# Performance work log

Measured on AMD Instinct MI355X. Metric: run time of the kernel, lower is better.

The kernel has to match this reference:

```python
import jax, jax.numpy as jnp
import numpy as np

D = 4096
N_HEAD = 32
KV_HEAD = 8
GS = D * KV_HEAD // N_HEAD  # 1024, kv projection width
B, S = 1, 2048


def setup_inputs() -> dict:
    key = jax.random.key(0)
    ks = jax.random.split(key, 10)
    sc = 0.02
    return {
        "x": jax.random.normal(ks[0], (B, S, D), dtype=jnp.float32),
        "y": jax.random.normal(ks[1], (B, S, D), dtype=jnp.float32),
        "Wq": jax.random.normal(ks[2], (D, D), dtype=jnp.float32) * sc,
        "bq": jax.random.normal(ks[3], (D,), dtype=jnp.float32) * sc,
        "Wk": jax.random.normal(ks[4], (D, GS), dtype=jnp.float32) * sc,
        "bk": jax.random.normal(ks[5], (GS,), dtype=jnp.float32) * sc,
        "Wv": jax.random.normal(ks[6], (D, GS), dtype=jnp.float32) * sc,
        "bv": jax.random.normal(ks[7], (GS,), dtype=jnp.float32) * sc,
        "Wo": jax.random.normal(ks[8], (D, D), dtype=jnp.float32) * sc,
        "bo": jax.random.normal(ks[9], (D,), dtype=jnp.float32) * sc,
        "n_head": N_HEAD,
        "kv_head": KV_HEAD,
    }


def reference(x, y, Wq, bq, Wk, bk, Wv, bv, Wo, bo, n_head, kv_head):
    b, s, d = x.shape
    hd = d // n_head              # per-head dim
    gvs = hd // 2                 # complex pairs per head (group_vector_size)
    q = (x @ Wq + bq).reshape(b, s, n_head, hd)
    k = (y @ Wk + bk).reshape(b, s, kv_head, hd)
    v = (y @ Wv + bv).reshape(b, s, kv_head, hd)

    # RoPE: phi = 1/5000**(i/gvs); angle[p, i] = phi[i] * p  (matrix.T in torch)
    phi = 1.0 / (5000.0 ** (jnp.arange(gvs, dtype=jnp.float32) / gvs))
    ang = jnp.arange(s, dtype=jnp.float32)[:, None] * phi[None, :]  # [S, gvs]
    cos = jnp.cos(ang)[None, :, None, :]  # [1,S,1,gvs]
    sin = jnp.sin(ang)[None, :, None, :]

    def rope(t):
        # interleaved pairs (t[...,2i], t[...,2i+1]) form complex numbers
        tr, ti = t[..., 0::2], t[..., 1::2]
        ro = tr * cos - ti * sin
        io = tr * sin + ti * cos
        return jnp.stack([ro, io], axis=-1).reshape(t.shape)

    q = rope(q)
    k = rope(k)

    # GQA: head h uses kv head h // (n_head // kv_head) -> repeat kv heads
    module = n_head // kv_head
    k = jnp.repeat(k, module, axis=2)  # [B,S,H,hd]
    v = jnp.repeat(v, module, axis=2)

    scores = jnp.einsum("bqhd,bkhd->bhqk", q, k) / jnp.sqrt(jnp.float32(hd))
    causal = jnp.tril(jnp.ones((s, s), dtype=bool))
    scores = jnp.where(causal[None, None], scores, -jnp.inf)
    attn = jax.nn.softmax(scores, axis=-1)
    out = jnp.einsum("bhqk,bkhd->bqhd", attn, v).reshape(b, s, d)
    return out @ Wo + bo
```

## Files before the change

### kernel.cpp

```cpp
#include <hip/hip_runtime.h>
#include <hip/hip_bf16.h>

typedef unsigned int uint32;
typedef unsigned short ushort16;
typedef __attribute__((ext_vector_type(8))) __bf16 bf16x8;
typedef __attribute__((ext_vector_type(4))) float f32x4;

__device__ __forceinline__ ushort16 f2bf(float f) {
    uint32 u = __float_as_uint(f);
    u += 0x7fff + ((u >> 16) & 1);
    return (ushort16)(u >> 16);
}
__device__ __forceinline__ uint32 pack2rn(float a, float b) {
    uint32 ua = __float_as_uint(a) + 0x8000u;
    uint32 ub = __float_as_uint(b) + 0x8000u;
    return __builtin_amdgcn_perm(ub, ua, 0x07060302);
}
__device__ __forceinline__ float blo(uint32 u) { return __uint_as_float(u << 16); }
__device__ __forceinline__ float bhi(uint32 u) { return __uint_as_float(u & 0xffff0000u); }

__device__ __forceinline__ void storeC(float v, float* p) { *p = v; }
__device__ __forceinline__ void storeC(float v, ushort16* p) { *p = f2bf(v); }

__device__ __forceinline__ void gload_lds16(const void* g, void* l) {
    __builtin_amdgcn_global_load_lds(
        (const __attribute__((address_space(1))) unsigned int*)g,
        (__attribute__((address_space(3))) unsigned int*)l, 16, 0, 0);
}

__global__ __launch_bounds__(256) void conv_bf16(
    const float* __restrict__ X, ushort16* __restrict__ Xb, int n8)
{
    int idx = blockIdx.x * blockDim.x + threadIdx.x;
    if (idx >= n8) return;
    float4 a = ((const float4*)X)[2 * idx];
    float4 b = ((const float4*)X)[2 * idx + 1];
    uint4 u;
    u.x = pack2rn(a.x, a.y); u.y = pack2rn(a.z, a.w);
    u.z = pack2rn(b.x, b.y); u.w = pack2rn(b.z, b.w);
    ((uint4*)Xb)[idx] = u;
}

__global__ __launch_bounds__(256) void transpose_w_bf16(
    const float* __restrict__ W, ushort16* __restrict__ Wt, int N)
{
    __shared__ float tile[64][65];
    const int k0 = blockIdx.x * 64, n0 = blockIdx.y * 64;
#pragma unroll
    for (int it = 0; it < 16; ++it) {
        int idx = threadIdx.x + it * 256;
        int r = idx >> 6, c = idx & 63;
        tile[r][c] = W[(size_t)(k0 + r) * N + n0 + c];
    }
    __syncthreads();
#pragma unroll
    for (int it = 0; it < 8; ++it) {
        int idx = threadIdx.x + it * 256;
        int nr = idx >> 5, kp = idx & 31;
        uint32 u = pack2rn(tile[2 * kp][nr], tile[2 * kp + 1][nr]);
        *(uint32*)&Wt[(size_t)(n0 + nr) * 4096 + k0 + 2 * kp] = u;
    }
}

template <typename OutT>
__global__ __launch_bounds__(256) void gemm_mfma(
    const ushort16* __restrict__ A, const ushort16* __restrict__ B,
    const float* __restrict__ b1, const float* __restrict__ b2,
    OutT* __restrict__ C, int N, int K, int nsplit)
{
    __shared__ __align__(16) ushort16 As[128 * 64];
    __shared__ __align__(16) ushort16 Bs[128 * 64];

    const int tid  = threadIdx.x;
    const int lane = tid & 63, wave = tid >> 6;
    const int quad = lane >> 4, m16 = lane & 15;
    const int wm = (wave >> 1) * 64, wn = (wave & 1) * 64;
    const int gm0 = blockIdx.y * 128, gn0 = blockIdx.x * 128;

    f32x4 acc[4][4];
#pragma unroll
    for (int i = 0; i < 4; ++i)
#pragma unroll
        for (int j = 0; j < 4; ++j) acc[i][j] = (f32x4){0.f, 0.f, 0.f, 0.f};

    const int rl = lane >> 3, cl = lane & 7;
    const int clog = cl ^ (rl & 7);
    const ushort16* Ag = A + (size_t)(gm0 + wave * 32 + rl) * K + clog * 8;
    const ushort16* Bg = B + (size_t)(gn0 + wave * 32 + rl) * K + clog * 8;
    char* AsW = (char*)As + wave * 4096;
    char* BsW = (char*)Bs + wave * 4096;

    for (int k0 = 0; k0 < K; k0 += 64) {
        __syncthreads();
#pragma unroll
        for (int i = 0; i < 4; ++i) {
            gload_lds16(Ag + (size_t)(8 * i) * K, AsW + i * 1024);
            gload_lds16(Bg + (size_t)(8 * i) * K, BsW + i * 1024);
        }
        Ag += 64; Bg += 64;
        __syncthreads();

#pragma unroll
        for (int s = 0; s < 2; ++s) {
            bf16x8 aF[4], bF[4];
            const int cr = s * 4 + quad;
#pragma unroll
            for (int i = 0; i < 4; ++i) {
                int r = wm + i * 16 + m16;
                aF[i] = *(const bf16x8*)&As[r * 64 + ((cr ^ (r & 7)) * 8)];
                int n = wn + i * 16 + m16;
                bF[i] = *(const bf16x8*)&Bs[n * 64 + ((cr ^ (n & 7)) * 8)];
            }
            __builtin_amdgcn_s_setprio(1);
#pragma unroll
            for (int i = 0; i < 4; ++i)
#pragma unroll
                for (int j = 0; j < 4; ++j)
                    acc[i][j] = __builtin_amdgcn_mfma_f32_16x16x32_bf16(
                        aF[i], bF[j], acc[i][j], 0, 0, 0);
            __builtin_amdgcn_s_setprio(0);
        }
    }

#pragma unroll
    for (int j = 0; j < 4; ++j) {
        int col = gn0 + wn + j * 16 + m16;
        float bb = (col < nsplit) ? b1[col] : b2[col - nsplit];
#pragma unroll
        for (int i = 0; i < 4; ++i) {
            int row0 = gm0 + wm + i * 16 + quad * 4;
#pragma unroll
            for (int r = 0; r < 4; ++r)
                storeC(acc[i][j][r] + bb, C + (size_t)(row0 + r) * N + col);
        }
    }
}

__global__ void rope_q_kernel(const float* __restrict__ T,
                              ushort16* __restrict__ Qb, int S)
{
    int idx = blockIdx.x * blockDim.x + threadIdx.x;
    if (idx >= S * 32 * 64) return;
    int i   = idx & 63;
    int rem = idx >> 6;
    int s   = rem >> 5;
    float inv = powf(5000.0f, -(float)i / 64.0f);
    float ang = (float)s * inv;
    float cs = cosf(ang), sn = sinf(ang);
    const float sc = 0.08838834764831845f * 1.4426950408889634f;
    size_t base = (size_t)rem * 128 + 2 * i;
    float tr = T[base], ti = T[base + 1];
    *(uint32*)&Qb[base] = pack2rn((tr * cs - ti * sn) * sc,
                                  (tr * sn + ti * cs) * sc);
}

__global__ void rope_k_kernel(ushort16* __restrict__ KVb, int S)
{
    int idx = blockIdx.x * blockDim.x + threadIdx.x;
    if (idx >= S * 8 * 64) return;
    int i   = idx & 63;
    int rem = idx >> 6;
    int s   = rem >> 3, h = rem & 7;
    float inv = powf(5000.0f, -(float)i / 64.0f);
    float ang = (float)s * inv;
    float cs = cosf(ang), sn = sinf(ang);
    uint32* p = (uint32*)&KVb[(size_t)s * 2048 + h * 128 + 2 * i];
    uint32 u = *p;
    float tr = blo(u), ti = bhi(u);
    *p = pack2rn(tr * cs - ti * sn, tr * sn + ti * cs);
}

__global__ __launch_bounds__(256) void flash_attn_kernel(
    const ushort16* __restrict__ Qb, const ushort16* __restrict__ KVb,
    ushort16* __restrict__ O)
{
    __shared__ __align__(16) ushort16 Ks[64 * 128];
    __shared__ __align__(16) ushort16 Vt[128 * 64];
    __shared__ __align__(16) ushort16 Ps[64 * 64];

    const int tid  = threadIdx.x;
    const int lane = tid & 63, wave = tid >> 6;
    const int quad = lane >> 4, m16 = lane & 15;
    const int h = (int)blockIdx.y, kvh = h >> 2;

    const ushort16* Kbase = KVb + kvh * 128;
    const ushort16* Vbase = KVb + 1024 + kvh * 128;

    for (int pass = 0; pass < 2; ++pass) {
        const int qi = pass ? (int)blockIdx.x : 31 - (int)blockIdx.x;
        const int q0 = qi * 64;

        bf16x8 qa[4];
        {
            const ushort16* qp = Qb + (size_t)(q0 + wave * 16 + m16) * 4096
                               + h * 128 + quad * 8;
#pragma unroll
            for (int ks = 0; ks < 4; ++ks)
                qa[ks] = *(const bf16x8*)(qp + ks * 32);
        }

        f32x4 acc_o[8];
#pragma unroll
        for (int t = 0; t < 8; ++t) acc_o[t] = (f32x4){0.f, 0.f, 0.f, 0.f};
        float m_i[4], l_i[4];
#pragma unroll
        for (int r = 0; r < 4; ++r) { m_i[r] = -1e30f; l_i[r] = 0.f; }

        for (int k0 = 0; k0 <= q0; k0 += 64) {
            __syncthreads();

#pragma unroll
            for (int it = 0; it < 4; ++it) {
                int idx = tid + it * 256;
                int row = idx >> 4, c = idx & 15;
                *(uint4*)&Ks[row * 128 + ((c ^ (row & 7)) * 8)] =
                    *(const uint4*)(Kbase + (size_t)(k0 + row) * 2048 + c * 8);
            }
#pragma unroll
            for (int it = 0; it < 2; ++it) {
                int idx = tid + it * 256;
                int rp  = idx & 31;
                int dcb = (idx >> 5) * 8;
                const ushort16* p0 = Vbase + (size_t)(k0 + 2 * rp) * 2048 + dcb;
                uint4 a = *(const uint4*)p0;
                uint4 b = *(const uint4*)(p0 + 2048);
                uint32 aw[4] = {a.x, a.y, a.z, a.w}, bw[4] = {b.x, b.y, b.z, b.w};
                int cc = rp >> 2, cbase = 2 * (rp & 3);
#pragma unroll
                for (int t = 0; t < 4; ++t) {
                    int d0 = dcb + 2 * t, d1 = d0 + 1;
                    *(uint32*)&Vt[d0 * 64 + ((cc ^ (d0 & 7)) * 8) + cbase] =
                        __builtin_amdgcn_perm(bw[t], aw[t], 0x05040100);
                    *(uint32*)&Vt[d1 * 64 + ((cc ^ (d1 & 7)) * 8) + cbase] =
                        __builtin_amdgcn_perm(bw[t], aw[t], 0x07060302);
                }
            }
            __syncthreads();

            f32x4 sacc[4];
#pragma unroll
            for (int j = 0; j < 4; ++j) sacc[j] = (f32x4){0.f, 0.f, 0.f, 0.f};
            __builtin_amdgcn_s_setprio(1);
#pragma unroll
            for (int ks = 0; ks < 4; ++ks) {
#pragma unroll
                for (int j = 0; j < 4; ++j) {
                    int n = j * 16 + m16;
                    bf16x8 kb = *(const bf16x8*)&Ks[n * 128 + (((ks * 4 + quad) ^ (n & 7)) * 8)];
                    sacc[j] = __builtin_amdgcn_mfma_f32_16x16x32_bf16(qa[ks], kb, sacc[j], 0, 0, 0);
                }
            }
            __builtin_amdgcn_s_setprio(0);

            if (k0 == q0) {
                int qr = wave * 16 + quad * 4;
#pragma unroll
                for (int j = 0; j < 4; ++j) {
                    int kvl = j * 16 + m16;
#pragma unroll
                    for (int r = 0; r < 4; ++r)
                        if (kvl > qr + r) sacc[j][r] = -1e30f;
                }
            }

#pragma unroll
            for (int r = 0; r < 4; ++r) {
                float rm = fmaxf(fmaxf(sacc[0][r], sacc[1][r]), fmaxf(sacc[2][r], sacc[3][r]));
                rm = fmaxf(rm, __shfl_xor(rm, 1));
                rm = fmaxf(rm, __shfl_xor(rm, 2));
                rm = fmaxf(rm, __shfl_xor(rm, 4));
                rm = fmaxf(rm, __shfl_xor(rm, 8));
                float mnew = fmaxf(m_i[r], rm);
                float al = exp2f(m_i[r] - mnew);
                float rs = 0.f;
#pragma unroll
                for (int j = 0; j < 4; ++j) {
                    float pv = exp2f(sacc[j][r] - mnew);
                    sacc[j][r] = pv;
                    rs += pv;
                }
                rs += __shfl_xor(rs, 1);
                rs += __shfl_xor(rs, 2);
                rs += __shfl_xor(rs, 4);
                rs += __shfl_xor(rs, 8);
                l_i[r] = l_i[r] * al + rs;
                m_i[r] = mnew;
                int q = wave * 16 + quad * 4 + r;
#pragma unroll
                for (int j = 0; j < 4; ++j) {
                    int kv = j * 16 + m16;
                    Ps[q * 64 + (((kv >> 3) ^ (q & 7)) * 8) + (kv & 7)] = f2bf(sacc[j][r]);
                }
#pragma unroll
                for (int t = 0; t < 8; ++t) acc_o[t][r] *= al;
            }

            int qrow = wave * 16 + m16;
#pragma unroll
            for (int ks2 = 0; ks2 < 2; ++ks2) {
                bf16x8 pa = *(const bf16x8*)&Ps[qrow * 64 + (((ks2 * 4 + quad) ^ (qrow & 7)) * 8)];
                __builtin_amdgcn_s_setprio(1);
#pragma unroll
                for (int t = 0; t < 8; ++t) {
                    int d = t * 16 + m16;
                    bf16x8 vb = *(const bf16x8*)&Vt[d * 64 + (((ks2 * 4 + quad) ^ (d & 7)) * 8)];
                    acc_o[t] = __builtin_amdgcn_mfma_f32_16x16x32_bf16(pa, vb, acc_o[t], 0, 0, 0);
                }
                __builtin_amdgcn_s_setprio(0);
            }
        }

        ushort16* op = O + (size_t)(q0 + wave * 16 + quad * 4) * 4096 + h * 128 + m16;
#pragma unroll
        for (int r = 0; r < 4; ++r) {
            float inv = 1.0f / l_i[r];
#pragma unroll
            for (int t = 0; t < 8; ++t)
                op[(size_t)r * 4096 + t * 16] = f2bf(acc_o[t][r] * inv);
        }
    }
}

extern "C" void kernel_launch(void* const* d_in, const int* in_sizes, int n_in,
                              void* d_out, int out_size, void* d_ws, size_t ws_size,
                              hipStream_t stream)
{
    const float* x  = (const float*)d_in[0];
    const float* y  = (const float*)d_in[1];
    const float* Wq = (const float*)d_in[2];
    const float* bq = (const float*)d_in[3];
    const float* Wk = (const float*)d_in[4];
    const float* bk = (const float*)d_in[5];
    const float* Wv = (const float*)d_in[6];
    const float* bv = (const float*)d_in[7];
    const float* Wo = (const float*)d_in[8];
    const float* bo = (const float*)d_in[9];
    float* out = (float*)d_out;

    const int S = 2048, D = 4096;
    const size_t MB = 1024 * 1024;

    char* ws = (char*)d_ws;
    ushort16* xb   = (ushort16*)(ws);
    ushort16* yb   = (ushort16*)(ws + 16 * MB);
    ushort16* Wqt  = (ushort16*)(ws + 32 * MB);
    ushort16* Wkvt = (ushort16*)(ws + 64 * MB);
    ushort16* Wot  = (ushort16*)(ws + 80 * MB);
    ushort16* KVb  = (ushort16*)(ws + 112 * MB);
    ushort16* Qb   = xb;
    ushort16* Ao   = yb;
    float*    Q    = out;

    const int n8 = S * D / 8;
    conv_bf16<<<n8 / 256, 256, 0, stream>>>(x, xb, n8);
    conv_bf16<<<n8 / 256, 256, 0, stream>>>(y, yb, n8);
    transpose_w_bf16<<<dim3(64, 64), 256, 0, stream>>>(Wq, Wqt, D);
    transpose_w_bf16<<<dim3(64, 16), 256, 0, stream>>>(Wk, Wkvt, 1024);
    transpose_w_bf16<<<dim3(64, 16), 256, 0, stream>>>(Wv, Wkvt + (size_t)1024 * 4096, 1024);
    transpose_w_bf16<<<dim3(64, 64), 256, 0, stream>>>(Wo, Wot, D);

    gemm_mfma<float><<<dim3(32, 16), 256, 0, stream>>>(
        xb, Wqt, bq, bq, Q, D, D, D);
    gemm_mfma<ushort16><<<dim3(16, 16), 256, 0, stream>>>(
        yb, Wkvt, bk, bv, KVb, 2048, D, 1024);

    rope_q_kernel<<<(S * 32 * 64 + 255) / 256, 256, 0, stream>>>(Q, Qb, S);
    rope_k_kernel<<<(S * 8 * 64 + 255) / 256, 256, 0, stream>>>(KVb, S);

    flash_attn_kernel<<<dim3(16, 32), 256, 0, stream>>>(Qb, KVb, Ao);

    gemm_mfma<float><<<dim3(32, 16), 256, 0, stream>>>(
        Ao, Wot, bo, bo, out, D, D, D);
}
```

Baseline: 664.9 us.

## Merge prep, QKV GEMM and RoPE launches; one query tile per attention block

Merges the x/y bf16 conversion into one launch and the Wq/Wk/Wv transposes into one launch. Replaces the separate Q and KV projection GEMMs with a single gemm_qkv launch that picks its operands by block index, and fuses the Q and K RoPE kernels into one. This removes launch gaps and lets the smaller KV GEMM share a wave with the Q GEMM. Flash attention now does one query tile per block on a 32x32 grid instead of two paired tiles per block on 16x32. That doubles the block count but drops the paired load balancing, so causal work per block becomes uneven.

```diff
diff --git a/kernel.cpp b/kernel.cpp
--- a/kernel.cpp
+++ b/kernel.cpp
@@ -28,24 +28,35 @@
         (__attribute__((address_space(3))) unsigned int*)l, 16, 0, 0);
 }
 
-__global__ __launch_bounds__(256) void conv_bf16(
-    const float* __restrict__ X, ushort16* __restrict__ Xb, int n8)
+__global__ __launch_bounds__(256) void conv2_bf16(
+    const float* __restrict__ X, const float* __restrict__ Y,
+    ushort16* __restrict__ Xb, ushort16* __restrict__ Yb, int n8)
 {
     int idx = blockIdx.x * blockDim.x + threadIdx.x;
-    if (idx >= n8) return;
-    float4 a = ((const float4*)X)[2 * idx];
-    float4 b = ((const float4*)X)[2 * idx + 1];
+    const float* S = (idx < n8) ? X : Y;
+    ushort16*    D = (idx < n8) ? Xb : Yb;
+    int i = (idx < n8) ? idx : idx - n8;
+    if (i >= n8) return;
+    float4 a = ((const float4*)S)[2 * i];
+    float4 b = ((const float4*)S)[2 * i + 1];
     uint4 u;
     u.x = pack2rn(a.x, a.y); u.y = pack2rn(a.z, a.w);
     u.z = pack2rn(b.x, b.y); u.w = pack2rn(b.z, b.w);
-    ((uint4*)Xb)[idx] = u;
+    ((uint4*)D)[i] = u;
 }
 
 __global__ __launch_bounds__(256) void transpose_w_bf16(
-    const float* __restrict__ W, ushort16* __restrict__ Wt, int N)
+    const float* __restrict__ Wq, const float* __restrict__ Wk,
+    const float* __restrict__ Wv, ushort16* __restrict__ Wqt,
+    ushort16* __restrict__ Wkvt)
 {
     __shared__ float tile[64][65];
-    const int k0 = blockIdx.x * 64, n0 = blockIdx.y * 64;
+    const int yb = blockIdx.y;
+    const float* W; ushort16* Wt; int N, n0;
+    if (yb < 64)      { W = Wq; Wt = Wqt;  N = 4096; n0 = yb * 64; }
+    else if (yb < 80) { W = Wk; Wt = Wkvt; N = 1024; n0 = (yb - 64) * 64; }
+    else              { W = Wv; Wt = Wkvt + (size_t)1024 * 4096; N = 1024; n0 = (yb - 80) * 64; }
+    const int k0 = blockIdx.x * 64;
 #pragma unroll
     for (int it = 0; it < 16; ++it) {
         int idx = threadIdx.x + it * 256;
@@ -62,20 +73,28 @@
     }
 }
 
-template <typename OutT>
-__global__ __launch_bounds__(256) void gemm_mfma(
-    const ushort16* __restrict__ A, const ushort16* __restrict__ B,
-    const float* __restrict__ b1, const float* __restrict__ b2,
-    OutT* __restrict__ C, int N, int K, int nsplit)
+__global__ __launch_bounds__(256) void gemm_qkv(
+    const ushort16* __restrict__ xb, const ushort16* __restrict__ yb,
+    const ushort16* __restrict__ Wqt, const ushort16* __restrict__ Wkvt,
+    const float* __restrict__ bq, const float* __restrict__ bk,
+    const float* __restrict__ bv, float* __restrict__ Q,
+    ushort16* __restrict__ KVb)
 {
     __shared__ __align__(16) ushort16 As[128 * 64];
     __shared__ __align__(16) ushort16 Bs[128 * 64];
+
+    const bool isQ = (blockIdx.x < 32);
+    const ushort16* A = isQ ? xb : yb;
+    const ushort16* B = isQ ? Wqt : Wkvt;
+    const int N   = isQ ? 4096 : 2048;
+    const int gn0 = (isQ ? (int)blockIdx.x : (int)blockIdx.x - 32) * 128;
+    const int gm0 = blockIdx.y * 128;
+    const int K = 4096;
 
     const int tid  = threadIdx.x;
     const int lane = tid & 63, wave = tid >> 6;
     const int quad = lane >> 4, m16 = lane & 15;
     const int wm = (wave >> 1) * 64, wn = (wave & 1) * 64;
-    const int gm0 = blockIdx.y * 128, gn0 = blockIdx.x * 128;
 
     f32x4 acc[4][4];
 #pragma unroll
@@ -125,49 +144,125 @@
 #pragma unroll
     for (int j = 0; j < 4; ++j) {
         int col = gn0 + wn + j * 16 + m16;
-        float bb = (col < nsplit) ? b1[col] : b2[col - nsplit];
+        float bb = isQ ? bq[col] : ((col < 1024) ? bk[col] : bv[col - 1024]);
 #pragma unroll
         for (int i = 0; i < 4; ++i) {
             int row0 = gm0 + wm + i * 16 + quad * 4;
 #pragma unroll
+            for (int r = 0; r < 4; ++r) {
+                float v = acc[i][j][r] + bb;
+                if (isQ) Q[(size_t)(row0 + r) * 4096 + col] = v;
+                else     KVb[(size_t)(row0 + r) * 2048 + col] = f2bf(v);
+            }
+        }
+    }
+}
+
+template <typename OutT>
+__global__ __launch_bounds__(256) void gemm_mfma(
+    const ushort16* __restrict__ A, const ushort16* __restrict__ B,
+    const float* __restrict__ b1, OutT* __restrict__ C, int N, int K)
+{
+    __shared__ __align__(16) ushort16 As[128 * 64];
+    __shared__ __align__(16) ushort16 Bs[128 * 64];
+
+    const int tid  = threadIdx.x;
+    const int lane = tid & 63, wave = tid >> 6;
+    const int quad = lane >> 4, m16 = lane & 15;
+    const int wm = (wave >> 1) * 64, wn = (wave & 1) * 64;
+    const int gm0 = blockIdx.y * 128, gn0 = blockIdx.x * 128;
+
+    f32x4 acc[4][4];
+#pragma unroll
+    for (int i = 0; i < 4; ++i)
+#pragma unroll
+        for (int j = 0; j < 4; ++j) acc[i][j] = (f32x4){0.f, 0.f, 0.f, 0.f};
+
+    const int rl = lane >> 3, cl = lane & 7;
+    const int clog = cl ^ (rl & 7);
+    const ushort16* Ag = A + (size_t)(gm0 + wave * 32 + rl) * K + clog * 8;
+    const ushort16* Bg = B + (size_t)(gn0 + wave * 32 + rl) * K + clog * 8;
+    char* AsW = (char*)As + wave * 4096;
+    char* BsW = (char*)Bs + wave * 4096;
+
+    for (int k0 = 0; k0 < K; k0 += 64) {
+        __syncthreads();
+#pragma unroll
+        for (int i = 0; i < 4; ++i) {
+            gload_lds16(Ag + (size_t)(8 * i) * K, AsW + i * 1024);
+            gload_lds16(Bg + (size_t)(8 * i) * K, BsW + i * 1024);
+        }
+        Ag += 64; Bg += 64;
+        __syncthreads();
+
+#pragma unroll
+        for (int s = 0; s < 2; ++s) {
+            bf16x8 aF[4], bF[4];
+            const int cr = s * 4 + quad;
+#pragma unroll
+            for (int i = 0; i < 4; ++i) {
+                int r = wm + i * 16 + m16;
+                aF[i] = *(const bf16x8*)&As[r * 64 + ((cr ^ (r & 7)) * 8)];
+                int n = wn + i * 16 + m16;
+                bF[i] = *(const bf16x8*)&Bs[n * 64 + ((cr ^ (n & 7)) * 8)];
+            }
+            __builtin_amdgcn_s_setprio(1);
+#pragma unroll
+            for (int i = 0; i < 4; ++i)
+#pragma unroll
+                for (int j = 0; j < 4; ++j)
+                    acc[i][j] = __builtin_amdgcn_mfma_f32_16x16x32_bf16(
+                        aF[i], bF[j], acc[i][j], 0, 0, 0);
+            __builtin_amdgcn_s_setprio(0);
+        }
+    }
+
+#pragma unroll
+    for (int j = 0; j < 4; ++j) {
+        int col = gn0 + wn + j * 16 + m16;
+        float bb = b1[col];
+#pragma unroll
+        for (int i = 0; i < 4; ++i) {
+            int row0 = gm0 + wm + i * 16 + quad * 4;
+#pragma unroll
             for (int r = 0; r < 4; ++r)
                 storeC(acc[i][j][r] + bb, C + (size_t)(row0 + r) * N + col);
         }
     }
 }
 
-__global__ void rope_q_kernel(const float* __restrict__ T,
-                              ushort16* __restrict__ Qb, int S)
+__global__ void rope_kernel(const float* __restrict__ T,
+                            ushort16* __restrict__ Qb,
+                            ushort16* __restrict__ KVb, int S)
 {
     int idx = blockIdx.x * blockDim.x + threadIdx.x;
-    if (idx >= S * 32 * 64) return;
-    int i   = idx & 63;
-    int rem = idx >> 6;
-    int s   = rem >> 5;
-    float inv = powf(5000.0f, -(float)i / 64.0f);
-    float ang = (float)s * inv;
-    float cs = cosf(ang), sn = sinf(ang);
-    const float sc = 0.08838834764831845f * 1.4426950408889634f;
-    size_t base = (size_t)rem * 128 + 2 * i;
-    float tr = T[base], ti = T[base + 1];
-    *(uint32*)&Qb[base] = pack2rn((tr * cs - ti * sn) * sc,
-                                  (tr * sn + ti * cs) * sc);
-}
-
-__global__ void rope_k_kernel(ushort16* __restrict__ KVb, int S)
-{
-    int idx = blockIdx.x * blockDim.x + threadIdx.x;
-    if (idx >= S * 8 * 64) return;
-    int i   = idx & 63;
-    int rem = idx >> 6;
-    int s   = rem >> 3, h = rem & 7;
-    float inv = powf(5000.0f, -(float)i / 64.0f);
-    float ang = (float)s * inv;
-    float cs = cosf(ang), sn = sinf(ang);
-    uint32* p = (uint32*)&KVb[(size_t)s * 2048 + h * 128 + 2 * i];
-    uint32 u = *p;
-    float tr = blo(u), ti = bhi(u);
-    *p = pack2rn(tr * cs - ti * sn, tr * sn + ti * cs);
+    const int nq = S * 32 * 64;
+    if (idx < nq) {
+        int i   = idx & 63;
+        int rem = idx >> 6;
+        int s   = rem >> 5;
+        float inv = powf(5000.0f, -(float)i / 64.0f);
+        float ang = (float)s * inv;
+        float cs = cosf(ang), sn = sinf(ang);
+        const float sc = 0.08838834764831845f * 1.4426950408889634f;
+        size_t base = (size_t)rem * 128 + 2 * i;
+        float tr = T[base], ti = T[base + 1];
+        *(uint32*)&Qb[base] = pack2rn((tr * cs - ti * sn) * sc,
+                                      (tr * sn + ti * cs) * sc);
+    } else {
+        idx -= nq;
+        if (idx >= S * 8 * 64) return;
+        int i   = idx & 63;
+        int rem = idx >> 6;
+        int s   = rem >> 3, h = rem & 7;
+        float inv = powf(5000.0f, -(float)i / 64.0f);
+        float ang = (float)s * inv;
+        float cs = cosf(ang), sn = sinf(ang);
+        uint32* p = (uint32*)&KVb[(size_t)s * 2048 + h * 128 + 2 * i];
+        uint32 u = *p;
+        float tr = blo(u), ti = bhi(u);
+        *p = pack2rn(tr * cs - ti * sn, tr * sn + ti * cs);
+    }
 }
 
 __global__ __launch_bounds__(256) void flash_attn_kernel(
@@ -181,143 +276,140 @@
     const int tid  = threadIdx.x;
     const int lane = tid & 63, wave = tid >> 6;
     const int quad = lane >> 4, m16 = lane & 15;
-    const int h = (int)blockIdx.y, kvh = h >> 2;
+    const int g = (int)blockIdx.y, h = g, kvh = h >> 2;
+    const int qi = (g & 16) ? (31 - (int)blockIdx.x) : (int)blockIdx.x;
+    const int q0 = qi * 64;
 
     const ushort16* Kbase = KVb + kvh * 128;
     const ushort16* Vbase = KVb + 1024 + kvh * 128;
 
-    for (int pass = 0; pass < 2; ++pass) {
-        const int qi = pass ? (int)blockIdx.x : 31 - (int)blockIdx.x;
-        const int q0 = qi * 64;
-
-        bf16x8 qa[4];
-        {
-            const ushort16* qp = Qb + (size_t)(q0 + wave * 16 + m16) * 4096
-                               + h * 128 + quad * 8;
-#pragma unroll
-            for (int ks = 0; ks < 4; ++ks)
-                qa[ks] = *(const bf16x8*)(qp + ks * 32);
-        }
-
-        f32x4 acc_o[8];
-#pragma unroll
-        for (int t = 0; t < 8; ++t) acc_o[t] = (f32x4){0.f, 0.f, 0.f, 0.f};
-        float m_i[4], l_i[4];
-#pragma unroll
-        for (int r = 0; r < 4; ++r) { m_i[r] = -1e30f; l_i[r] = 0.f; }
-
-        for (int k0 = 0; k0 <= q0; k0 += 64) {
-            __syncthreads();
-
-#pragma unroll
-            for (int it = 0; it < 4; ++it) {
-                int idx = tid + it * 256;
-                int row = idx >> 4, c = idx & 15;
-                *(uint4*)&Ks[row * 128 + ((c ^ (row & 7)) * 8)] =
-                    *(const uint4*)(Kbase + (size_t)(k0 + row) * 2048 + c * 8);
-            }
-#pragma unroll
-            for (int it = 0; it < 2; ++it) {
-                int idx = tid + it * 256;
-                int rp  = idx & 31;
-                int dcb = (idx >> 5) * 8;
-                const ushort16* p0 = Vbase + (size_t)(k0 + 2 * rp) * 2048 + dcb;
-                uint4 a = *(const uint4*)p0;
-                uint4 b = *(const uint4*)(p0 + 2048);
-                uint32 aw[4] = {a.x, a.y, a.z, a.w}, bw[4] = {b.x, b.y, b.z, b.w};
-                int cc = rp >> 2, cbase = 2 * (rp & 3);
-#pragma unroll
-                for (int t = 0; t < 4; ++t) {
-                    int d0 = dcb + 2 * t, d1 = d0 + 1;
-                    *(uint32*)&Vt[d0 * 64 + ((cc ^ (d0 & 7)) * 8) + cbase] =
-                        __builtin_amdgcn_perm(bw[t], aw[t], 0x05040100);
-                    *(uint32*)&Vt[d1 * 64 + ((cc ^ (d1 & 7)) * 8) + cbase] =
-                        __builtin_amdgcn_perm(bw[t], aw[t], 0x07060302);
-                }
-            }
-            __syncthreads();
-
-            f32x4 sacc[4];
-#pragma unroll
-            for (int j = 0; j < 4; ++j) sacc[j] = (f32x4){0.f, 0.f, 0.f, 0.f};
+    bf16x8 qa[4];
+    {
+        const ushort16* qp = Qb + (size_t)(q0 + wave * 16 + m16) * 4096
+                           + h * 128 + quad * 8;
+#pragma unroll
+        for (int ks = 0; ks < 4; ++ks)
+            qa[ks] = *(const bf16x8*)(qp + ks * 32);
+    }
+
+    f32x4 acc_o[8];
+#pragma unroll
+    for (int t = 0; t < 8; ++t) acc_o[t] = (f32x4){0.f, 0.f, 0.f, 0.f};
+    float m_i[4], l_i[4];
+#pragma unroll
+    for (int r = 0; r < 4; ++r) { m_i[r] = -1e30f; l_i[r] = 0.f; }
+
+    for (int k0 = 0; k0 <= q0; k0 += 64) {
+        __syncthreads();
+
+#pragma unroll
+        for (int it = 0; it < 4; ++it) {
+            int idx = tid + it * 256;
+            int row = idx >> 4, c = idx & 15;
+            *(uint4*)&Ks[row * 128 + ((c ^ (row & 7)) * 8)] =
+                *(const uint4*)(Kbase + (size_t)(k0 + row) * 2048 + c * 8);
+        }
+#pragma unroll
+        for (int it = 0; it < 2; ++it) {
+            int idx = tid + it * 256;
+            int rp  = idx & 31;
+            int dcb = (idx >> 5) * 8;
+            const ushort16* p0 = Vbase + (size_t)(k0 + 2 * rp) * 2048 + dcb;
+            uint4 a = *(const uint4*)p0;
+            uint4 b = *(const uint4*)(p0 + 2048);
+            uint32 aw[4] = {a.x, a.y, a.z, a.w}, bw[4] = {b.x, b.y, b.z, b.w};
+            int cc = rp >> 2, cbase = 2 * (rp & 3);
+#pragma unroll
+            for (int t = 0; t < 4; ++t) {
+                int d0 = dcb + 2 * t, d1 = d0 + 1;
+                *(uint32*)&Vt[d0 * 64 + ((cc ^ (d0 & 7)) * 8) + cbase] =
+                    __builtin_amdgcn_perm(bw[t], aw[t], 0x05040100);
+                *(uint32*)&Vt[d1 * 64 + ((cc ^ (d1 & 7)) * 8) + cbase] =
+                    __builtin_amdgcn_perm(bw[t], aw[t], 0x07060302);
+            }
+        }
+        __syncthreads();
+
+        f32x4 sacc[4];
+#pragma unroll
+        for (int j = 0; j < 4; ++j) sacc[j] = (f32x4){0.f, 0.f, 0.f, 0.f};
+        __builtin_amdgcn_s_setprio(1);
+#pragma unroll
+        for (int ks = 0; ks < 4; ++ks) {
+#pragma unroll
+            for (int j = 0; j < 4; ++j) {
+                int n = j * 16 + m16;
+                bf16x8 kb = *(const bf16x8*)&Ks[n * 128 + (((ks * 4 + quad) ^ (n & 7)) * 8)];
+                sacc[j] = __builtin_amdgcn_mfma_f32_16x16x32_bf16(qa[ks], kb, sacc[j], 0, 0, 0);
+            }
+        }
+        __builtin_amdgcn_s_setprio(0);
+
+        if (k0 == q0) {
+            int qr = wave * 16 + quad * 4;
+#pragma unroll
+            for (int j = 0; j < 4; ++j) {
+                int kvl = j * 16 + m16;
+#pragma unroll
+                for (int r = 0; r < 4; ++r)
+                    if (kvl > qr + r) sacc[j][r] = -1e30f;
+            }
+        }
+
+#pragma unroll
+        for (int r = 0; r < 4; ++r) {
+            float rm = fmaxf(fmaxf(sacc[0][r], sacc[1][r]), fmaxf(sacc[2][r], sacc[3][r]));
+            rm = fmaxf(rm, __shfl_xor(rm, 1));
+            rm = fmaxf(rm, __shfl_xor(rm, 2));
+            rm = fmaxf(rm, __shfl_xor(rm, 4));
+            rm = fmaxf(rm, __shfl_xor(rm, 8));
+            float mnew = fmaxf(m_i[r], rm);
+            float al = exp2f(m_i[r] - mnew);
+            float rs = 0.f;
+#pragma unroll
+            for (int j = 0; j < 4; ++j) {
+                float pv = exp2f(sacc[j][r] - mnew);
+                sacc[j][r] = pv;
+                rs += pv;
+            }
+            rs += __shfl_xor(rs, 1);
+            rs += __shfl_xor(rs, 2);
+            rs += __shfl_xor(rs, 4);
+            rs += __shfl_xor(rs, 8);
+            l_i[r] = l_i[r] * al + rs;
+            m_i[r] = mnew;
+            int q = wave * 16 + quad * 4 + r;
+#pragma unroll
+            for (int j = 0; j < 4; ++j) {
+                int kv = j * 16 + m16;
+                Ps[q * 64 + (((kv >> 3) ^ (q & 7)) * 8) + (kv & 7)] = f2bf(sacc[j][r]);
+            }
+#pragma unroll
+            for (int t = 0; t < 8; ++t) acc_o[t][r] *= al;
+        }
+
+        int qrow = wave * 16 + m16;
+#pragma unroll
+        for (int ks2 = 0; ks2 < 2; ++ks2) {
+            bf16x8 pa = *(const bf16x8*)&Ps[qrow * 64 + (((ks2 * 4 + quad) ^ (qrow & 7)) * 8)];
             __builtin_amdgcn_s_setprio(1);
 #pragma unroll
-            for (int ks = 0; ks < 4; ++ks) {
-#pragma unroll
-                for (int j = 0; j < 4; ++j) {
-                    int n = j * 16 + m16;
-                    bf16x8 kb = *(const bf16x8*)&Ks[n * 128 + (((ks * 4 + quad) ^ (n & 7)) * 8)];
-                    sacc[j] = __builtin_amdgcn_mfma_f32_16x16x32_bf16(qa[ks], kb, sacc[j], 0, 0, 0);
-                }
+            for (int t = 0; t < 8; ++t) {
+                int d = t * 16 + m16;
+                bf16x8 vb = *(const bf16x8*)&Vt[d * 64 + (((ks2 * 4 + quad) ^ (d & 7)) * 8)];
+                acc_o[t] = __builtin_amdgcn_mfma_f32_16x16x32_bf16(pa, vb, acc_o[t], 0, 0, 0);
             }
             __builtin_amdgcn_s_setprio(0);
-
-            if (k0 == q0) {
-                int qr = wave * 16 + quad * 4;
-#pragma unroll
-                for (int j = 0; j < 4; ++j) {
-                    int kvl = j * 16 + m16;
-#pragma unroll
-                    for (int r = 0; r < 4; ++r)
-                        if (kvl > qr + r) sacc[j][r] = -1e30f;
-                }
-            }
-
-#pragma unroll
-            for (int r = 0; r < 4; ++r) {
-                float rm = fmaxf(fmaxf(sacc[0][r], sacc[1][r]), fmaxf(sacc[2][r], sacc[3][r]));
-                rm = fmaxf(rm, __shfl_xor(rm, 1));
-                rm = fmaxf(rm, __shfl_xor(rm, 2));
-                rm = fmaxf(rm, __shfl_xor(rm, 4));
-                rm = fmaxf(rm, __shfl_xor(rm, 8));
-                float mnew = fmaxf(m_i[r], rm);
-                float al = exp2f(m_i[r] - mnew);
-                float rs = 0.f;
-#pragma unroll
-                for (int j = 0; j < 4; ++j) {
-                    float pv = exp2f(sacc[j][r] - mnew);
-                    sacc[j][r] = pv;
-                    rs += pv;
-                }
-                rs += __shfl_xor(rs, 1);
-                rs += __shfl_xor(rs, 2);
-                rs += __shfl_xor(rs, 4);
-                rs += __shfl_xor(rs, 8);
-                l_i[r] = l_i[r] * al + rs;
-                m_i[r] = mnew;
-                int q = wave * 16 + quad * 4 + r;
-#pragma unroll
-                for (int j = 0; j < 4; ++j) {
-                    int kv = j * 16 + m16;
-                    Ps[q * 64 + (((kv >> 3) ^ (q & 7)) * 8) + (kv & 7)] = f2bf(sacc[j][r]);
-                }
-#pragma unroll
-                for (int t = 0; t < 8; ++t) acc_o[t][r] *= al;
-            }
-
-            int qrow = wave * 16 + m16;
-#pragma unroll
-            for (int ks2 = 0; ks2 < 2; ++ks2) {
-                bf16x8 pa = *(const bf16x8*)&Ps[qrow * 64 + (((ks2 * 4 + quad) ^ (qrow & 7)) * 8)];
-                __builtin_amdgcn_s_setprio(1);
-#pragma unroll
-                for (int t = 0; t < 8; ++t) {
-                    int d = t * 16 + m16;
-                    bf16x8 vb = *(const bf16x8*)&Vt[d * 64 + (((ks2 * 4 + quad) ^ (d & 7)) * 8)];
-                    acc_o[t] = __builtin_amdgcn_mfma_f32_16x16x32_bf16(pa, vb, acc_o[t], 0, 0, 0);
-                }
-                __builtin_amdgcn_s_setprio(0);
-            }
-        }
-
-        ushort16* op = O + (size_t)(q0 + wave * 16 + quad * 4) * 4096 + h * 128 + m16;
-#pragma unroll
-        for (int r = 0; r < 4; ++r) {
-            float inv = 1.0f / l_i[r];
-#pragma unroll
-            for (int t = 0; t < 8; ++t)
-                op[(size_t)r * 4096 + t * 16] = f2bf(acc_o[t][r] * inv);
-        }
+        }
+    }
+
+    ushort16* op = O + (size_t)(q0 + wave * 16 + quad * 4) * 4096 + h * 128 + m16;
+#pragma unroll
+    for (int r = 0; r < 4; ++r) {
+        float inv = 1.0f / l_i[r];
+#pragma unroll
+        for (int t = 0; t < 8; ++t)
+            op[(size_t)r * 4096 + t * 16] = f2bf(acc_o[t][r] * inv);
     }
 }
 
@@ -352,23 +444,19 @@
     float*    Q    = out;
 
     const int n8 = S * D / 8;
-    conv_bf16<<<n8 / 256, 256, 0, stream>>>(x, xb, n8);
-    conv_bf16<<<n8 / 256, 256, 0, stream>>>(y, yb, n8);
-    transpose_w_bf16<<<dim3(64, 64), 256, 0, stream>>>(Wq, Wqt, D);
-    transpose_w_bf16<<<dim3(64, 16), 256, 0, stream>>>(Wk, Wkvt, 1024);
-    transpose_w_bf16<<<dim3(64, 16), 256, 0, stream>>>(Wv, Wkvt + (size_t)1024 * 4096, 1024);
-    transpose_w_bf16<<<dim3(64, 64), 256, 0, stream>>>(Wo, Wot, D);
+    conv2_bf16<<<2 * n8 / 256, 256, 0, stream>>>(x, y, xb, yb, n8);
+    transpose_w_bf16<<<dim3(64, 96), 256, 0, stream>>>(Wq, Wk, Wv, Wqt, Wkvt);
+    {
+    }
+    transpose_w_bf16<<<dim3(64, 64), 256, 0, stream>>>(Wo, Wk, Wv, Wot, Wkvt + (size_t)2048 * 4096);
+
+    gemm_qkv<<<dim3(48, 16), 256, 0, stream>>>(
+        xb, yb, Wqt, Wkvt, bq, bk, bv, Q, KVb);
+
+    rope_kernel<<<(S * 40 * 64) / 256, 256, 0, stream>>>(Q, Qb, KVb, S);
+
+    flash_attn_kernel<<<dim3(32, 32), 256, 0, stream>>>(Qb, KVb, Ao);
 
     gemm_mfma<float><<<dim3(32, 16), 256, 0, stream>>>(
-        xb, Wqt, bq, bq, Q, D, D, D);
-    gemm_mfma<ushort16><<<dim3(16, 16), 256, 0, stream>>>(
-        yb, Wkvt, bk, bv, KVb, 2048, D, 1024);
-
-    rope_q_kernel<<<(S * 32 * 64 + 255) / 256, 256, 0, stream>>>(Q, Qb, S);
-    rope_k_kernel<<<(S * 8 * 64 + 255) / 256, 256, 0, stream>>>(KVb, S);
-
-    flash_attn_kernel<<<dim3(16, 32), 256, 0, stream>>>(Qb, KVb, Ao);
-
-    gemm_mfma<float><<<dim3(32, 16), 256, 0, stream>>>(
-        Ao, Wot, bo, bo, out, D, D, D);
-}
+        Ao, Wot, bo, out, D, D);
+}
```

Result: slower. 706.0 us (+6.2%).
